# Performance work log

Hardware: AMD Instinct MI355X
Metric: run time of the kernel (lower is better)

Reference implementation:

```python
import jax, jax.numpy as jnp
import numpy as np
import math

N_HEADS = 8
NUM_LAYERS = 2
OUT_LEN = 96
MIN_FACTOR, MAX_FACTOR = 3, 10
MIN_KERNEL, MAX_KERNEL = 5, 51
LN_EPS = 1e-5


def layer_norm(x, g, b):
    mu = x.mean(-1, keepdims=True)
    var = x.var(-1, keepdims=True)  # biased, like nn.LayerNorm
    return (x - mu) / jnp.sqrt(var + LN_EPS) * g + b


def prob_sparse_attn(x, wq, bq, wk, bk, wv, bv, wo, bo):
    B, L, D = x.shape
    H, dk = N_HEADS, D // N_HEADS
    Q = (x @ wq + bq).reshape(B, L, H, dk).transpose(0, 2, 1, 3)  # [B,H,L,dk]
    K = (x @ wk + bk).reshape(B, L, H, dk).transpose(0, 2, 1, 3)
    V = (x @ wv + bv).reshape(B, L, H, dk).transpose(0, 2, 1, 3)
    # sparsity score per query: 0.5*||q|| + 0.3*entropy(softmax(q)) + 0.2*var(q)
    l2 = jnp.linalg.norm(Q, axis=-1)
    prob = jax.nn.softmax(Q, axis=-1)
    ent = -jnp.sum(prob * jnp.log(prob + 1e-9), axis=-1)
    var = Q.var(axis=-1, ddof=1)  # torch.var unbiased
    qs = 0.5 * l2 + 0.3 * ent + 0.2 * var  # [B,H,L]
    std = qs.std(axis=2, ddof=1)
    mean = qs.mean(axis=2)
    factor = jnp.clip(jnp.round(std / (mean + 1e-6) * MAX_FACTOR), MIN_FACTOR, MAX_FACTOR).astype(jnp.int32)  # [B,H]
    u = factor[:, 0]  # torch uses k_list[b][0]: head-0 factor per batch
    umax = min(MAX_FACTOR, L)
    _, top_idx = jax.lax.top_k(qs, umax)  # [B,H,umax]
    keep = jnp.arange(umax)[None, None, :] < u[:, None, None]  # [B,1->H,umax]
    Qs = jnp.take_along_axis(Q, top_idx[..., None], axis=2)  # [B,H,umax,dk]
    scores = jnp.einsum('bhud,bhld->bhul', Qs, K) / math.sqrt(dk)
    attn = jax.nn.softmax(scores, axis=-1)
    out = jnp.einsum('bhul,bhld->bhud', attn, V)  # [B,H,umax,dk]
    # scatter selected query outputs back; rows beyond u[b] are dropped (OOB index L)
    idx = jnp.where(keep, top_idx, L)
    full = jnp.zeros((B, H, L, dk), x.dtype)
    bI = jnp.arange(B)[:, None, None]
    hI = jnp.arange(H)[None, :, None]
    full = full.at[bI, hI, idx].set(out, mode='drop')
    y = full.transpose(0, 2, 1, 3).reshape(B, L, D)
    return y @ wo + bo


def adaptive_decomp(x):
    B, L, D = x.shape
    spec = jnp.abs(jnp.fft.rfft(x, axis=1)).mean(axis=(0, 2))
    peak = jnp.argmax(spec[1:]) + 1
    period = jnp.clip(L // peak, MIN_KERNEL, MAX_KERNEL)
    period = jnp.where(period % 2 == 0, period + 1, period)
    pad = period // 2
    # avg_pool1d(kernel=period, stride=1, padding=pad, count_include_pad=False) via cumsum
    t = jnp.arange(L)
    start = jnp.clip(t - pad, 0, L)
    end = jnp.clip(t + pad + 1, 0, L)
    cs = jnp.concatenate([jnp.zeros((B, 1, D), x.dtype), jnp.cumsum(x, axis=1)], axis=1)
    cnt = (end - start).astype(x.dtype)[None, :, None]
    trend = (cs[:, end] - cs[:, start]) / cnt
    return x - trend, trend


def _forward(x, w_embed, b_embed, wq, bq, wk, bk, wv, bv, wo, bo,
             w1, b1, w2, b2, g1, beta1, g2, beta2, w_out, b_out):
    h = x @ w_embed + b_embed
    for _ in range(NUM_LAYERS):  # share_params=True: same weights each layer
        a = prob_sparse_attn(h, wq, bq, wk, bk, wv, bv, wo, bo)
        h = layer_norm(h + a, g1, beta1)
        ffn = jax.nn.relu(h @ w1 + b1) @ w2 + b2
        h = layer_norm(h + ffn, g2, beta2)
    seasonal, trend = adaptive_decomp(h)
    combined = seasonal + trend
    out_seq = combined[:, -OUT_LEN:, :]
    pred = (out_seq @ w_out + b_out)[..., 0]  # [B, OUT_LEN]
    return pred


def setup_inputs() -> dict:
    key = jax.random.key(0)
    ks = jax.random.split(key, 16)
    B, L, Din, D, Dff = 16, 4096, 8, 512, 2048
    w = lambda k, shp: (jax.random.normal(k, shp, jnp.float32) * 0.02)
    return {
        'x': jax.random.normal(ks[0], (B, L, Din), jnp.float32),
        'w_embed': w(ks[1], (Din, D)), 'b_embed': jnp.zeros((D,), jnp.float32),
        'wq': w(ks[2], (D, D)), 'bq': jnp.zeros((D,), jnp.float32),
        'wk': w(ks[3], (D, D)), 'bk': jnp.zeros((D,), jnp.float32),
        'wv': w(ks[4], (D, D)), 'bv': jnp.zeros((D,), jnp.float32),
        'wo': w(ks[5], (D, D)), 'bo': jnp.zeros((D,), jnp.float32),
        'w1': w(ks[6], (D, Dff)), 'b1': jnp.zeros((Dff,), jnp.float32),
        'w2': w(ks[7], (Dff, D)), 'b2': jnp.zeros((D,), jnp.float32),
        'g1': jnp.ones((D,), jnp.float32), 'beta1': jnp.zeros((D,), jnp.float32),
        'g2': jnp.ones((D,), jnp.float32), 'beta2': jnp.zeros((D,), jnp.float32),
        'w_out': w(ks[8], (D, 1)), 'b_out': jnp.zeros((1,), jnp.float32),
    }


def reference(x, w_embed, b_embed, wq, bq, wk, bk, wv, bv, wo, bo,
              w1, b1, w2, b2, g1, beta1, g2, beta2, w_out, b_out):
    return _forward(x, w_embed, b_embed, wq, bq, wk, bk, wv, bv, wo, bo,
                    w1, b1, w2, b2, g1, beta1, g2, beta2, w_out, b_out)
```

## Files before the change

### kernel.cpp

```cpp
#include <hip/hip_runtime.h>
#include <math.h>

#define BB 16
#define LL 4096
#define DIN 8
#define DD 512
#define HH 8
#define DKK 64
#define DFF 2048
#define OUTLEN 96
#define TAIL0 (LL - OUTLEN)
#define NTAIL (BB * OUTLEN)
#define UMAX 10
#define CH 8192
#define QKVN 1536
#define NB 4
#define QM (NB * LL)
#define NSPLIT 32
#define LCHUNK (LL / NSPLIT)
#define PSTRIDE 68
#define MAXSLOT 128

typedef unsigned short ushort_t;
typedef unsigned int uint_t;
typedef short bf16x8 __attribute__((ext_vector_type(8)));
typedef float f32x4 __attribute__((ext_vector_type(4)));

#define GLD16(gp, lp) __builtin_amdgcn_global_load_lds((const __attribute__((address_space(1))) void*)(gp), (__attribute__((address_space(3))) void*)(lp), 16, 0, 0)

__device__ inline float wsum(float v){
#pragma unroll
  for (int o = 32; o > 0; o >>= 1) v += __shfl_xor(v, o);
  return v;
}
__device__ inline float wmax(float v){
#pragma unroll
  for (int o = 32; o > 0; o >>= 1) v = fmaxf(v, __shfl_xor(v, o));
  return v;
}
__device__ inline ushort_t f2bf_rtn(float f){
  uint_t u = __float_as_uint(f);
  uint_t r = u + 0x7FFF + ((u >> 16) & 1);
  return (ushort_t)(r >> 16);
}
__device__ inline float bf2f(ushort_t u){
  return __uint_as_float(((uint_t)u) << 16);
}
__device__ inline void split2(float x, ushort_t& hi, ushort_t& lo){
  uint_t u = __float_as_uint(x);
  hi = (ushort_t)(u >> 16);
  lo = f2bf_rtn(x - __uint_as_float(u & 0xFFFF0000u));
}

__global__ __launch_bounds__(256) void embed_kernel(const float* __restrict__ x,
    const float* __restrict__ we, const float* __restrict__ be,
    ushort_t* __restrict__ hh, ushort_t* __restrict__ hl){
  int row = blockIdx.x;
  __shared__ float xs[DIN];
  if (threadIdx.x < DIN) xs[threadIdx.x] = x[(size_t)row * DIN + threadIdx.x];
  __syncthreads();
  for (int j = threadIdx.x; j < DD; j += 256){
    float acc = be[j];
#pragma unroll
    for (int i = 0; i < DIN; ++i) acc += xs[i] * we[i * DD + j];
    ushort_t hu, lu; split2(acc, hu, lu);
    hh[(size_t)row * DD + j] = hu;
    hl[(size_t)row * DD + j] = lu;
  }
}

__global__ __launch_bounds__(256) void wsplit_t_kernel(const float* __restrict__ W,
    ushort_t* __restrict__ Th, ushort_t* __restrict__ Tl, int K, int N){
  int idx = blockIdx.x * 256 + threadIdx.x;
  if (idx >= N * K) return;
  int n = idx / K, k = idx - n * K;
  ushort_t hi, lo;
  split2(W[(size_t)k * N + n], hi, lo);
  Th[idx] = hi; Tl[idx] = lo;
}
__global__ __launch_bounds__(256) void wqkv_prep_kernel(const float* __restrict__ wq,
    const float* __restrict__ wk, const float* __restrict__ wv,
    ushort_t* __restrict__ Th, ushort_t* __restrict__ Tl){
  int idx = blockIdx.x * 256 + threadIdx.x;
  if (idx >= QKVN * DD) return;
  int n = idx >> 9, k = idx & (DD - 1);
  const float* src = (n < 512) ? wq : (n < 1024) ? wk : wv;
  ushort_t hi, lo;
  split2(src[(size_t)k * DD + (n & 511)], hi, lo);
  Th[idx] = hi; Tl[idx] = lo;
}
__global__ __launch_bounds__(256) void bqkv_prep_kernel(const float* __restrict__ bq,
    const float* __restrict__ bk, const float* __restrict__ bv, float* __restrict__ bo_){
  int n = blockIdx.x * 256 + threadIdx.x;
  if (n >= QKVN) return;
  bo_[n] = (n < 512) ? bq[n] : (n < 1024) ? bk[n - 512] : bv[n - 1024];
}

__global__ __launch_bounds__(256) void gemm_qkv(
    const ushort_t* __restrict__ Ah, const ushort_t* __restrict__ Al,
    const ushort_t* __restrict__ Bh, const ushort_t* __restrict__ Bl,
    const float* __restrict__ bias, float* __restrict__ Q,
    ushort_t* __restrict__ KV){
  __shared__ __align__(16) ushort_t AsH[128 * 32];
  __shared__ __align__(16) ushort_t AsL[128 * 32];
  __shared__ __align__(16) ushort_t BsH[128 * 32];
  __shared__ __align__(16) ushort_t BsL[128 * 32];
  const int tid  = threadIdx.x;
  const int lane = tid & 63;
  const int wv   = tid >> 6;
  const int m0   = blockIdx.y * 128;
  const int n0   = blockIdx.x * 128;
  const bool isQ = (n0 < 512);
  const int wm   = (wv & 1) * 64;
  const int wn   = (wv >> 1) * 64;

  const int rowA = tid >> 2;
  const int qe   = (tid & 3) * 8;
  const int lds0 = tid * 8;
  const int lds1 = (tid + 256) * 8;

  f32x4 acc[4][4];
#pragma unroll
  for (int i = 0; i < 4; ++i)
#pragma unroll
    for (int j = 0; j < 4; ++j) acc[i][j] = (f32x4){0.f, 0.f, 0.f, 0.f};

  const int arow = lane & 15;
  const int koff = (lane >> 4) * 8;
  const int K = DD;

  for (int k0 = 0; k0 < K; k0 += 32){
    const size_t ga0 = (size_t)(m0 + rowA) * K + k0 + qe;
    const size_t ga1 = (size_t)(m0 + rowA + 64) * K + k0 + qe;
    const size_t gb0 = (size_t)(n0 + rowA) * K + k0 + qe;
    const size_t gb1 = (size_t)(n0 + rowA + 64) * K + k0 + qe;
    GLD16(Ah + ga0, &AsH[lds0]);  GLD16(Ah + ga1, &AsH[lds1]);
    GLD16(Al + ga0, &AsL[lds0]);  GLD16(Al + ga1, &AsL[lds1]);
    GLD16(Bh + gb0, &BsH[lds0]);  GLD16(Bh + gb1, &BsH[lds1]);
    if (isQ){ GLD16(Bl + gb0, &BsL[lds0]);  GLD16(Bl + gb1, &BsL[lds1]); }
    __syncthreads();

    bf16x8 ah[4], al[4], bh[4], bl[4];
#pragma unroll
    for (int i = 0; i < 4; ++i){
      ah[i] = *(const bf16x8*)&AsH[(wm + i * 16 + arow) * 32 + koff];
      al[i] = *(const bf16x8*)&AsL[(wm + i * 16 + arow) * 32 + koff];
      bh[i] = *(const bf16x8*)&BsH[(wn + i * 16 + arow) * 32 + koff];
      if (isQ) bl[i] = *(const bf16x8*)&BsL[(wn + i * 16 + arow) * 32 + koff];
    }
#pragma unroll
    for (int i = 0; i < 4; ++i)
#pragma unroll
      for (int j = 0; j < 4; ++j){
        acc[i][j] = __builtin_amdgcn_mfma_f32_16x16x32_bf16(ah[i], bh[j], acc[i][j], 0, 0, 0);
        acc[i][j] = __builtin_amdgcn_mfma_f32_16x16x32_bf16(al[i], bh[j], acc[i][j], 0, 0, 0);
        if (isQ)
          acc[i][j] = __builtin_amdgcn_mfma_f32_16x16x32_bf16(ah[i], bl[j], acc[i][j], 0, 0, 0);
      }
    __syncthreads();
  }

  const int crow = (lane >> 4) * 4;
  const int ccol = lane & 15;
#pragma unroll
  for (int i = 0; i < 4; ++i){
    const int gr0 = m0 + wm + i * 16 + crow;
#pragma unroll
    for (int j = 0; j < 4; ++j){
      const int gc = n0 + wn + j * 16 + ccol;
      const float bvv = bias[gc];
#pragma unroll
      for (int r = 0; r < 4; ++r){
        float v = acc[i][j][r] + bvv;
        const int gr = gr0 + r;
        if (isQ) Q[(size_t)gr * 512 + gc] = v;
        else     KV[(size_t)gr * 1024 + (gc - 512)] = f2bf_rtn(v);
      }
    }
  }
}

__global__ __launch_bounds__(256) void gemm_ffn1(
    const ushort_t* __restrict__ Ah, const ushort_t* __restrict__ Al,
    const ushort_t* __restrict__ Bh, const float* __restrict__ bias,
    ushort_t* __restrict__ Chid){
  __shared__ __align__(16) ushort_t AsH[128 * 32];
  __shared__ __align__(16) ushort_t AsL[128 * 32];
  __shared__ __align__(16) ushort_t BsH[128 * 32];
  const int tid  = threadIdx.x;
  const int lane = tid & 63;
  const int wv   = tid >> 6;
  const int m0   = blockIdx.y * 128;
  const int n0   = blockIdx.x * 128;
  const int wm   = (wv & 1) * 64;
  const int wn   = (wv >> 1) * 64;
  const int rowA = tid >> 2;
  const int qe   = (tid & 3) * 8;
  const int lds0 = tid * 8;
  const int lds1 = (tid + 256) * 8;

  f32x4 acc[4][4];
#pragma unroll
  for (int i = 0; i < 4; ++i)
#pragma unroll
    for (int j = 0; j < 4; ++j) acc[i][j] = (f32x4){0.f, 0.f, 0.f, 0.f};

  const int arow = lane & 15;
  const int koff = (lane >> 4) * 8;
  const int K = DD;

  for (int k0 = 0; k0 < K; k0 += 32){
    const size_t ga0 = (size_t)(m0 + rowA) * K + k0 + qe;
    const size_t ga1 = (size_t)(m0 + rowA + 64) * K + k0 + qe;
    const size_t gb0 = (size_t)(n0 + rowA) * K + k0 + qe;
    const size_t gb1 = (size_t)(n0 + rowA + 64) * K + k0 + qe;
    GLD16(Ah + ga0, &AsH[lds0]);  GLD16(Ah + ga1, &AsH[lds1]);
    GLD16(Al + ga0, &AsL[lds0]);  GLD16(Al + ga1, &AsL[lds1]);
    GLD16(Bh + gb0, &BsH[lds0]);  GLD16(Bh + gb1, &BsH[lds1]);
    __syncthreads();

    bf16x8 ah[4], al[4], bh[4];
#pragma unroll
    for (int i = 0; i < 4; ++i){
      ah[i] = *(const bf16x8*)&AsH[(wm + i * 16 + arow) * 32 + koff];
      al[i] = *(const bf16x8*)&AsL[(wm + i * 16 + arow) * 32 + koff];
      bh[i] = *(const bf16x8*)&BsH[(wn + i * 16 + arow) * 32 + koff];
    }
#pragma unroll
    for (int i = 0; i < 4; ++i)
#pragma unroll
      for (int j = 0; j < 4; ++j){
        acc[i][j] = __builtin_amdgcn_mfma_f32_16x16x32_bf16(ah[i], bh[j], acc[i][j], 0, 0, 0);
        acc[i][j] = __builtin_amdgcn_mfma_f32_16x16x32_bf16(al[i], bh[j], acc[i][j], 0, 0, 0);
      }
    __syncthreads();
  }

  const int crow = (lane >> 4) * 4;
  const int ccol = lane & 15;
#pragma unroll
  for (int i = 0; i < 4; ++i){
    const int gr0 = m0 + wm + i * 16 + crow;
#pragma unroll
    for (int j = 0; j < 4; ++j){
      const int gc = n0 + wn + j * 16 + ccol;
      const float bvv = bias[gc];
#pragma unroll
      for (int r = 0; r < 4; ++r){
        float v = fmaxf(acc[i][j][r] + bvv, 0.f);
        Chid[(size_t)(gr0 + r) * DFF + gc] = f2bf_rtn(v);
      }
    }
  }
}

__global__ __launch_bounds__(256) void gemm_ffn2(
    const ushort_t* __restrict__ Ahid,
    const ushort_t* __restrict__ Bh, const ushort_t* __restrict__ Bl,
    float* __restrict__ pbuf, size_t pstr){
  __shared__ __align__(16) ushort_t AsH[128 * 32];
  __shared__ __align__(16) ushort_t BsH[128 * 32];
  __shared__ __align__(16) ushort_t BsL[128 * 32];
  const int tid  = threadIdx.x;
  const int lane = tid & 63;
  const int wv   = tid >> 6;
  const int nblk = (int)blockIdx.x >> 1;
  const int kq   = (int)blockIdx.x & 1;
  const int m0   = blockIdx.y * 128;
  const int n0   = nblk * 128;
  const int wm   = (wv & 1) * 64;
  const int wn   = (wv >> 1) * 64;
  const int rowA = tid >> 2;
  const int qe   = (tid & 3) * 8;
  const int lds0 = tid * 8;
  const int lds1 = (tid + 256) * 8;

  f32x4 acc[4][4];
#pragma unroll
  for (int i = 0; i < 4; ++i)
#pragma unroll
    for (int j = 0; j < 4; ++j) acc[i][j] = (f32x4){0.f, 0.f, 0.f, 0.f};

  const int arow = lane & 15;
  const int koff = (lane >> 4) * 8;
  const int K = DFF;
  const int kper = K / 2;
  const int kbeg = kq * kper;

  for (int k0 = kbeg; k0 < kbeg + kper; k0 += 32){
    const size_t ga0 = (size_t)(m0 + rowA) * K + k0 + qe;
    const size_t ga1 = (size_t)(m0 + rowA + 64) * K + k0 + qe;
    const size_t gb0 = (size_t)(n0 + rowA) * K + k0 + qe;
    const size_t gb1 = (size_t)(n0 + rowA + 64) * K + k0 + qe;
    GLD16(Ahid + ga0, &AsH[lds0]);  GLD16(Ahid + ga1, &AsH[lds1]);
    GLD16(Bh + gb0, &BsH[lds0]);    GLD16(Bh + gb1, &BsH[lds1]);
    GLD16(Bl + gb0, &BsL[lds0]);    GLD16(Bl + gb1, &BsL[lds1]);
    __syncthreads();

    bf16x8 ah[4], bh[4], bl[4];
#pragma unroll
    for (int i = 0; i < 4; ++i){
      ah[i] = *(const bf16x8*)&AsH[(wm + i * 16 + arow) * 32 + koff];
      bh[i] = *(const bf16x8*)&BsH[(wn + i * 16 + arow) * 32 + koff];
      bl[i] = *(const bf16x8*)&BsL[(wn + i * 16 + arow) * 32 + koff];
    }
#pragma unroll
    for (int i = 0; i < 4; ++i)
#pragma unroll
      for (int j = 0; j < 4; ++j){
        acc[i][j] = __builtin_amdgcn_mfma_f32_16x16x32_bf16(ah[i], bh[j], acc[i][j], 0, 0, 0);
        acc[i][j] = __builtin_amdgcn_mfma_f32_16x16x32_bf16(ah[i], bl[j], acc[i][j], 0, 0, 0);
      }
    __syncthreads();
  }

  const int crow = (lane >> 4) * 4;
  const int ccol = lane & 15;
#pragma unroll
  for (int i = 0; i < 4; ++i){
    const int gr0 = m0 + wm + i * 16 + crow;
#pragma unroll
    for (int j = 0; j < 4; ++j){
      const int gc = n0 + wn + j * 16 + ccol;
#pragma unroll
      for (int r = 0; r < 4; ++r)
        pbuf[(size_t)kq * pstr + (size_t)(gr0 + r) * DD + gc] = acc[i][j][r];
    }
  }
}

__global__ __launch_bounds__(256) void qs_kernel(const float* __restrict__ qbuf, float* __restrict__ qsb){
  int tid = threadIdx.x;
  int lane = tid & 63;
  int wv = tid >> 6;
  int rid = blockIdx.x * 4 + wv;
  int bloc = rid >> 15;
  int hh = (rid >> 12) & 7;
  int l  = rid & (LL - 1);
  float qv = qbuf[((size_t)bloc * LL + l) * DD + hh * DKK + lane];
  float l2 = sqrtf(wsum(qv * qv));
  float mx = wmax(qv);
  float e  = expf(qv - mx);
  float se = wsum(e);
  float p  = e / se;
  float ent = -wsum(p * logf(p + 1e-9f));
  float mu  = wsum(qv) * (1.0f / 64.0f);
  float dv  = qv - mu;
  float var = wsum(dv * dv) * (1.0f / 63.0f);
  float val = 0.5f * l2 + 0.3f * ent + 0.2f * var;
  if (lane == 0) qsb[(size_t)(bloc * HH + hh) * LL + l] = val;
}

__global__ __launch_bounds__(256) void select_kernel(const float* __restrict__ qsb,
    int* __restrict__ topidx, int* __restrict__ ufac, int qtr){
  __shared__ float vals[LL];
  __shared__ float bv[256];
  __shared__ int   bi[256];
  __shared__ double r1[256], r2[256];
  const int bloc = blockIdx.y;
  const int b = qtr * NB + bloc;
  int tid = threadIdx.x;
  if (blockIdx.x == 8){
    const float* row = qsb + (size_t)bloc * HH * LL;
    double s = 0.0, s2 = 0.0;
    for (int l = tid; l < LL; l += 256){ double v = row[l]; s += v; s2 += v * v; }
    r1[tid] = s; r2[tid] = s2; __syncthreads();
    for (int st = 128; st; st >>= 1){
      if (tid < st){ r1[tid] += r1[tid+st]; r2[tid] += r2[tid+st]; }
      __syncthreads();
    }
    if (tid == 0){
      double mean = r1[0] / (double)LL;
      double var  = (r2[0] - (double)LL * mean * mean) / (double)(LL - 1);
      if (var < 0.0) var = 0.0;
      double f = rint(sqrt(var) / (mean + 1e-6) * 10.0);
      if (f < 3.0) f = 3.0;
      if (f > 10.0) f = 10.0;
      ufac[b] = (int)f;
    }
    return;
  }
  int hh = blockIdx.x;
  const float* row = qsb + ((size_t)bloc * HH + hh) * LL;
  for (int l = tid; l < LL; l += 256) vals[l] = row[l];
  __syncthreads();
  for (int it = 0; it < UMAX; ++it){
    float best = -INFINITY; int bidx = 0;
    for (int l = tid; l < LL; l += 256){
      float v = vals[l];
      if (v > best){ best = v; bidx = l; }
    }
    bv[tid] = best; bi[tid] = bidx; __syncthreads();
    for (int st = 128; st; st >>= 1){
      if (tid < st){
        if (bv[tid+st] > bv[tid] || (bv[tid+st] == bv[tid] && bi[tid+st] < bi[tid])){
          bv[tid] = bv[tid+st]; bi[tid] = bi[tid+st];
        }
      }
      __syncthreads();
    }
    if (tid == 0){ topidx[(b * HH + hh) * UMAX + it] = bi[0]; vals[bi[0]] = -INFINITY; }
    __syncthreads();
  }
}

__global__ void initslot_kernel(int* __restrict__ slotmap, int* __restrict__ scount){
  int i = blockIdx.x * 256 + threadIdx.x;
  if (i < BB * LL) slotmap[i] = -1;
  if (i < BB) scount[i] = 0;
}
__global__ __launch_bounds__(128) void slotbuild_kernel(const int* __restrict__ topidx,
    const int* __restrict__ ufac, int* __restrict__ slotmap, int* __restrict__ scount, int qtr){
  int t = threadIdx.x;
  int b = qtr * NB + blockIdx.x;
  if (t >= HH * UMAX) return;
  int hh = t / UMAX, rank = t % UMAX;
  if (rank >= ufac[b]) return;
  int qpos = topidx[(b * HH + hh) * UMAX + rank];
  int* cell = &slotmap[b * LL + qpos];
  int old = atomicCAS(cell, -1, -2);
  if (old == -1){
    int s = atomicAdd(&scount[b], 1);
    atomicExch(cell, s);
  }
}

__global__ __launch_bounds__(256) void attn_p1_kernel(const float* __restrict__ qbuf,
    const ushort_t* __restrict__ kvbuf,
    const int* __restrict__ topidx, const int* __restrict__ ufac,
    float* __restrict__ part, int qtr, int lmin){
  const int bloc = blockIdx.z;
  const int b = qtr * NB + bloc;
  const int rowid = blockIdx.y;
  const int hh = rowid / UMAX, rank = rowid % UMAX;
  if (rank >= ufac[b]) return;
  const int qpos = topidx[(b * HH + hh) * UMAX + rank];
  if (qpos < lmin) return;

  const int tid = threadIdx.x, lane = tid & 63, wv = tid >> 6;
  const int base = blockIdx.x * LCHUNK + wv * (LCHUNK / 4);

  __shared__ float qrow[DKK];
  __shared__ float wm4[4], ws4[4];
  __shared__ float pvs[4][DKK];
  if (tid < DKK) qrow[tid] = qbuf[((size_t)bloc * LL + qpos) * DD + hh * DKK + tid];
  __syncthreads();

  const ushort_t* Kp = kvbuf + (size_t)bloc * LL * 1024 + hh * DKK;
  const ushort_t* Vp = Kp + 512;
  const float qv = qrow[lane];

  float sc[32];
  float mloc = -INFINITY;
#pragma unroll
  for (int i = 0; i < 32; ++i){
    float s = wsum(qv * bf2f(Kp[(size_t)(base + i) * 1024 + lane])) * 0.125f;
    sc[i] = s;
    mloc = fmaxf(mloc, s);
  }
  if (lane == 0) wm4[wv] = mloc;
  __syncthreads();
  const float M4 = fmaxf(fmaxf(wm4[0], wm4[1]), fmaxf(wm4[2], wm4[3]));

  float ssum = 0.f;
#pragma unroll
  for (int i = 0; i < 32; ++i){ float e = expf(sc[i] - M4); sc[i] = e; ssum += e; }

  float pv = 0.f;
#pragma unroll
  for (int i = 0; i < 32; ++i) pv += sc[i] * bf2f(Vp[(size_t)(base + i) * 1024 + lane]);

  pvs[wv][lane] = pv;
  if (lane == 0) ws4[wv] = ssum;
  __syncthreads();
  if (wv == 0){
    float* rec = part + (size_t)((bloc * HH * UMAX + rowid) * NSPLIT + blockIdx.x) * PSTRIDE;
    rec[lane] = pvs[0][lane] + pvs[1][lane] + pvs[2][lane] + pvs[3][lane];
    if (lane == 0){ rec[64] = M4; rec[65] = ws4[0] + ws4[1] + ws4[2] + ws4[3]; }
  }
}

__global__ __launch_bounds__(256) void attn_p2_kernel(const float* __restrict__ part,
    const float* __restrict__ wo, const int* __restrict__ topidx, const int* __restrict__ ufac,
    const int* __restrict__ slotmap, float* __restrict__ adelta, int qtr, int lmin){
  const int bloc = blockIdx.y;
  const int b = qtr * NB + bloc;
  const int rowid = blockIdx.x;
  const int hh = rowid / UMAX, rank = rowid % UMAX;
  if (rank >= ufac[b]) return;
  const int qpos = topidx[(b * HH + hh) * UMAX + rank];
  if (qpos < lmin) return;
  const int slot = slotmap[b * LL + qpos];

  const int tid = threadIdx.x;
  const float* pbase = part + (size_t)(bloc * HH * UMAX + rowid) * NSPLIT * PSTRIDE;
  __shared__ float pm[NSPLIT], ps[NSPLIT];
  __shared__ float orow[DKK];
  if (tid < NSPLIT){
    pm[tid] = pbase[(size_t)tid * PSTRIDE + 64];
    ps[tid] = pbase[(size_t)tid * PSTRIDE + 65];
  }
  __syncthreads();
  float M = -INFINITY;
#pragma unroll
  for (int i = 0; i < NSPLIT; ++i) M = fmaxf(M, pm[i]);
  float S = 0.f;
#pragma unroll
  for (int i = 0; i < NSPLIT; ++i) S += ps[i] * expf(pm[i] - M);
  if (tid < DKK){
    float acc = 0.f;
#pragma unroll
    for (int i = 0; i < NSPLIT; ++i)
      acc += pbase[(size_t)i * PSTRIDE + tid] * expf(pm[i] - M);
    orow[tid] = acc / S;
  }
  __syncthreads();
  float* drow = adelta + ((size_t)b * MAXSLOT + slot) * DD;
  for (int j = tid; j < DD; j += 256){
    float a = 0.f;
#pragma unroll
    for (int dd = 0; dd < DKK; ++dd) a += orow[dd] * wo[(size_t)(hh * DKK + dd) * DD + j];
    atomicAdd(&drow[j], a);
  }
}

__global__ void zero_kernel(float* __restrict__ p, size_t n){
  size_t i = (size_t)blockIdx.x * 256 + threadIdx.x;
  size_t stride = (size_t)gridDim.x * 256;
  for (; i < n; i += stride) p[i] = 0.f;
}

template<bool TAIL>
__global__ __launch_bounds__(256) void ln1_kernel(
    const ushort_t* __restrict__ hh_, const ushort_t* __restrict__ hl_,
    const float* __restrict__ bo,
    const int* __restrict__ slotmap, const float* __restrict__ adelta,
    ushort_t* __restrict__ oh, ushort_t* __restrict__ ol,
    const float* __restrict__ g, const float* __restrict__ bb){
  __shared__ float red[256];
  int r = blockIdx.x, tid = threadIdx.x;
  int b, l;
  if (TAIL){ b = r / OUTLEN; l = TAIL0 + (r % OUTLEN); }
  else     { b = r >> 12;    l = r & (LL - 1); }
  const size_t gi = ((size_t)b * LL + l) * DD;
  float v0 = bf2f(hh_[gi + tid])       + bf2f(hl_[gi + tid])       + bo[tid];
  float v1 = bf2f(hh_[gi + tid + 256]) + bf2f(hl_[gi + tid + 256]) + bo[tid + 256];
  int s = slotmap[b * LL + l];
  if (s >= 0){
    const float* dr = adelta + ((size_t)b * MAXSLOT + s) * DD;
    v0 += dr[tid]; v1 += dr[tid + 256];
  }
  red[tid] = v0 + v1; __syncthreads();
  for (int st = 128; st; st >>= 1){ if (tid < st) red[tid] += red[tid+st]; __syncthreads(); }
  float mu = red[0] * (1.0f / DD); __syncthreads();
  float d0 = v0 - mu, d1 = v1 - mu;
  red[tid] = d0*d0 + d1*d1; __syncthreads();
  for (int st = 128; st; st >>= 1){ if (tid < st) red[tid] += red[tid+st]; __syncthreads(); }
  float rstd = rsqrtf(red[0] * (1.0f / DD) + 1e-5f);
  float o0 = d0 * rstd * g[tid]       + bb[tid];
  float o1 = d1 * rstd * g[tid + 256] + bb[tid + 256];
  const size_t oo = TAIL ? (size_t)r * DD : gi;
  ushort_t hu, lu;
  split2(o0, hu, lu); oh[oo + tid] = hu;       ol[oo + tid] = lu;
  split2(o1, hu, lu); oh[oo + tid + 256] = hu; ol[oo + tid + 256] = lu;
}

template<bool TAIL>
__global__ __launch_bounds__(256) void ln2_kernel(
    const ushort_t* __restrict__ ih, const ushort_t* __restrict__ il,
    const float* __restrict__ pbuf, size_t pstr, const float* __restrict__ b2,
    ushort_t* __restrict__ oh, ushort_t* __restrict__ ol, float* __restrict__ ofp,
    const float* __restrict__ g, const float* __restrict__ bb, size_t rowoff){
  __shared__ float red[256];
  int r = blockIdx.x, tid = threadIdx.x;
  const size_t gi = (rowoff + r) * DD;
  const size_t pi = (size_t)r * DD;
  float v0 = bf2f(ih[gi + tid]) + bf2f(il[gi + tid])
           + pbuf[pi + tid] + pbuf[pstr + pi + tid] + b2[tid];
  float v1 = bf2f(ih[gi + tid + 256]) + bf2f(il[gi + tid + 256])
           + pbuf[pi + tid + 256] + pbuf[pstr + pi + tid + 256] + b2[tid + 256];
  red[tid] = v0 + v1; __syncthreads();
  for (int st = 128; st; st >>= 1){ if (tid < st) red[tid] += red[tid+st]; __syncthreads(); }
  float mu = red[0] * (1.0f / DD); __syncthreads();
  float d0 = v0 - mu, d1 = v1 - mu;
  red[tid] = d0*d0 + d1*d1; __syncthreads();
  for (int st = 128; st; st >>= 1){ if (tid < st) red[tid] += red[tid+st]; __syncthreads(); }
  float rstd = rsqrtf(red[0] * (1.0f / DD) + 1e-5f);
  float o0 = d0 * rstd * g[tid]       + bb[tid];
  float o1 = d1 * rstd * g[tid + 256] + bb[tid + 256];
  if (TAIL){
    ofp[pi + tid] = o0; ofp[pi + tid + 256] = o1;
  } else {
    ushort_t hu, lu;
    split2(o0, hu, lu); oh[gi + tid] = hu;       ol[gi + tid] = lu;
    split2(o1, hu, lu); oh[gi + tid + 256] = hu; ol[gi + tid + 256] = lu;
  }
}

__global__ __launch_bounds__(64) void pred_kernel(const float* __restrict__ ht,
    const float* __restrict__ wout, const float* __restrict__ bout, float* __restrict__ out){
  int r = blockIdx.x, lane = threadIdx.x;
  float acc = 0.f;
  for (int dd = lane; dd < DD; dd += 64) acc += ht[(size_t)r * DD + dd] * wout[dd];
  acc = wsum(acc);
  if (lane == 0) out[r] = acc + bout[0];
}

extern "C" void kernel_launch(void* const* d_in, const int* in_sizes, int n_in,
                              void* d_out, int out_size, void* d_ws, size_t ws_size,
                              hipStream_t stream){
  const float* x    = (const float*)d_in[0];
  const float* wemb = (const float*)d_in[1];
  const float* bemb = (const float*)d_in[2];
  const float* wq   = (const float*)d_in[3];
  const float* bq   = (const float*)d_in[4];
  const float* wk   = (const float*)d_in[5];
  const float* bk   = (const float*)d_in[6];
  const float* wv   = (const float*)d_in[7];
  const float* bvv  = (const float*)d_in[8];
  const float* wo   = (const float*)d_in[9];
  const float* bo   = (const float*)d_in[10];
  const float* w1   = (const float*)d_in[11];
  const float* b1   = (const float*)d_in[12];
  const float* w2   = (const float*)d_in[13];
  const float* b2   = (const float*)d_in[14];
  const float* g1   = (const float*)d_in[15];
  const float* be1  = (const float*)d_in[16];
  const float* g2   = (const float*)d_in[17];
  const float* be2  = (const float*)d_in[18];
  const float* wout = (const float*)d_in[19];
  const float* bout = (const float*)d_in[20];
  float* out = (float*)d_out;
  char* wsb  = (char*)d_ws;

  const size_t MiB = 1024 * 1024;
  const size_t NE  = (size_t)BB * LL * DD;

  size_t o = 0;
  ushort_t* hh    = (ushort_t*)(wsb + o); o += NE * 2;
  ushort_t* hl    = (ushort_t*)(wsb + o); o += NE * 2;
  char*     arena = wsb + o;              o += 64 * MiB;
  float*    qbuf  = (float*)arena;
  ushort_t* kvbuf = (ushort_t*)(arena + 32 * MiB);
  ushort_t* hid   = (ushort_t*)arena;
  float*    pbuf  = (float*)(arena + 32 * MiB);
  ushort_t* hidt  = (ushort_t*)arena;
  float*    pbuft = (float*)(arena + 32 * MiB);
  ushort_t* asht  = (ushort_t*)(arena + 48 * MiB);
  ushort_t* aslt  = (ushort_t*)(arena + 50 * MiB);
  ushort_t* wtqkvh = (ushort_t*)(wsb + o); o += (size_t)QKVN * DD * 2;
  ushort_t* wtqkvl = (ushort_t*)(wsb + o); o += (size_t)QKVN * DD * 2;
  ushort_t* w1th   = (ushort_t*)(wsb + o); o += (size_t)DFF * DD * 2;
  ushort_t* w2th   = (ushort_t*)(wsb + o); o += (size_t)DD * DFF * 2;
  ushort_t* w2tl   = (ushort_t*)(wsb + o); o += (size_t)DD * DFF * 2;
  ushort_t* w1tl   = (ushort_t*)(wsb + o); o += (size_t)DFF * DD * 2;
  float*    bqkv   = (float*)(wsb + o);  o += QKVN * 4;
  float*    qsb    = (float*)(wsb + o);  o += (size_t)NB * HH * LL * 4;
  float*    part   = (float*)(wsb + o);  o += (size_t)NB * HH * UMAX * NSPLIT * PSTRIDE * 4;
  float*    adelta = (float*)(wsb + o);  o += (size_t)BB * MAXSLOT * DD * 4;
  float*    htail  = (float*)(wsb + o);  o += (size_t)NTAIL * DD * 4;
  int*      slotmap= (int*)(wsb + o);    o += (size_t)BB * LL * 4;
  int*      scount = (int*)(wsb + o);    o += BB * 4;
  int*      topidx = (int*)(wsb + o);    o += (size_t)BB * HH * UMAX * 4;
  int*      ufac   = (int*)(wsb + o);    o += 64;

  wqkv_prep_kernel<<<(QKVN*DD + 255)/256, 256, 0, stream>>>(wq, wk, wv, wtqkvh, wtqkvl);
  bqkv_prep_kernel<<<(QKVN + 255)/256, 256, 0, stream>>>(bq, bk, bvv, bqkv);
  wsplit_t_kernel<<<(DFF*DD + 255)/256, 256, 0, stream>>>(w1, w1th, w1tl, DD, DFF);
  wsplit_t_kernel<<<(DD*DFF + 255)/256, 256, 0, stream>>>(w2, w2th, w2tl, DFF, DD);

  embed_kernel<<<BB * LL, 256, 0, stream>>>(x, wemb, bemb, hh, hl);

  for (int layer = 0; layer < 2; ++layer){
    const bool tail = (layer == 1);
    const int lmin = tail ? TAIL0 : 0;

    initslot_kernel<<<(BB*LL + 255)/256, 256, 0, stream>>>(slotmap, scount);
    zero_kernel<<<1024, 256, 0, stream>>>(adelta, (size_t)BB * MAXSLOT * DD);

    for (int qtr = 0; qtr < BB / NB; ++qtr){
      const size_t hoff = (size_t)qtr * QM * DD;
      gemm_qkv<<<dim3(QKVN/128, QM/128), 256, 0, stream>>>(
          hh + hoff, hl + hoff, wtqkvh, wtqkvl, bqkv, qbuf, kvbuf);
      qs_kernel<<<(NB*HH*LL)/4, 256, 0, stream>>>(qbuf, qsb);
      select_kernel<<<dim3(9, NB), 256, 0, stream>>>(qsb, topidx, ufac, qtr);
      slotbuild_kernel<<<NB, 128, 0, stream>>>(topidx, ufac, slotmap, scount, qtr);
      attn_p1_kernel<<<dim3(NSPLIT, HH*UMAX, NB), 256, 0, stream>>>(
          qbuf, kvbuf, topidx, ufac, part, qtr, lmin);
      attn_p2_kernel<<<dim3(HH*UMAX, NB), 256, 0, stream>>>(
          part, wo, topidx, ufac, slotmap, adelta, qtr, lmin);
    }

    if (!tail){
      ln1_kernel<false><<<BB*LL, 256, 0, stream>>>(hh, hl, bo, slotmap, adelta, hh, hl, g1, be1);
      for (int c = 0; c < (BB*LL)/CH; ++c){
        const size_t roff = (size_t)c * CH;
        gemm_ffn1<<<dim3(DFF/128, CH/128), 256, 0, stream>>>(
            hh + roff * DD, hl + roff * DD, w1th, b1, hid);
        gemm_ffn2<<<dim3(8, CH/128), 256, 0, stream>>>(hid, w2th, w2tl, pbuf, (size_t)CH * DD);
        ln2_kernel<false><<<CH, 256, 0, stream>>>(
            hh, hl, pbuf, (size_t)CH * DD, b2, hh, hl, nullptr, g2, be2, roff);
      }
    } else {
      ln1_kernel<true><<<NTAIL, 256, 0, stream>>>(hh, hl, bo, slotmap, adelta, asht, aslt, g1, be1);
      gemm_ffn1<<<dim3(DFF/128, NTAIL/128), 256, 0, stream>>>(asht, aslt, w1th, b1, hidt);
      gemm_ffn2<<<dim3(8, NTAIL/128), 256, 0, stream>>>(hidt, w2th, w2tl, pbuft, (size_t)NTAIL * DD);
      ln2_kernel<true><<<NTAIL, 256, 0, stream>>>(
          asht, aslt, pbuft, (size_t)NTAIL * DD, b2, nullptr, nullptr, htail, g2, be2, 0);
      pred_kernel<<<NTAIL, 64, 0, stream>>>(htail, wout, bout, out);
    }
  }
  (void)in_sizes; (void)n_in; (void)out_size; (void)ws_size;
}
```

Measured before the change: 2.583 ms.

## Add XCD-aware block swizzle, reuse K/V across queries, vectorize LN and embed

Adds an XCD-aware workgroup remapping to the three GEMM kernels so neighbouring tiles share the same L2 on the MI355X's multiple compute dies. The attention partial kernel now loads each head's K/V chunk into registers once and loops over the selected query ranks, instead of launching one block per rank that re-reads K/V. The top-k selection keeps per-thread running maxima and rescans only the thread that owned the removed element, avoiding a full rescan per iteration. LayerNorm and embed kernels switch to packed 2-element loads and stores. The costs are more register pressure in the attention kernel and serialization across ranks inside a block.

```diff
diff --git a/kernel.cpp b/kernel.cpp
--- a/kernel.cpp
+++ b/kernel.cpp
@@ -51,6 +51,15 @@
   hi = (ushort_t)(u >> 16);
   lo = f2bf_rtn(x - __uint_as_float(u & 0xFFFF0000u));
 }
+__device__ inline void xcd_map(int& bx, int& by){
+  const int gx = gridDim.x;
+  const int nwg = gx * gridDim.y;
+  const int wg = (int)blockIdx.y * gx + (int)blockIdx.x;
+  const int q = nwg >> 3, r = nwg & 7;
+  const int xcd = wg & 7, idx = wg >> 3;
+  const int swz = (xcd < r ? xcd * (q + 1) : r * (q + 1) + (xcd - r) * q) + idx;
+  bx = swz % gx; by = swz / gx;
+}
 
 __global__ __launch_bounds__(256) void embed_kernel(const float* __restrict__ x,
     const float* __restrict__ we, const float* __restrict__ be,
@@ -59,14 +68,18 @@
   __shared__ float xs[DIN];
   if (threadIdx.x < DIN) xs[threadIdx.x] = x[(size_t)row * DIN + threadIdx.x];
   __syncthreads();
-  for (int j = threadIdx.x; j < DD; j += 256){
-    float acc = be[j];
-#pragma unroll
-    for (int i = 0; i < DIN; ++i) acc += xs[i] * we[i * DD + j];
-    ushort_t hu, lu; split2(acc, hu, lu);
-    hh[(size_t)row * DD + j] = hu;
-    hl[(size_t)row * DD + j] = lu;
-  }
+  const int t = threadIdx.x;
+  const int j0 = 2 * t;
+  float a0 = be[j0], a1 = be[j0 + 1];
+#pragma unroll
+  for (int i = 0; i < DIN; ++i){
+    a0 += xs[i] * we[i * DD + j0];
+    a1 += xs[i] * we[i * DD + j0 + 1];
+  }
+  ushort_t h0, l0, h1, l1;
+  split2(a0, h0, l0); split2(a1, h1, l1);
+  ((uint_t*)(hh + (size_t)row * DD))[t] = (uint_t)h0 | ((uint_t)h1 << 16);
+  ((uint_t*)(hl + (size_t)row * DD))[t] = (uint_t)l0 | ((uint_t)l1 << 16);
 }
 
 __global__ __launch_bounds__(256) void wsplit_t_kernel(const float* __restrict__ W,
@@ -105,11 +118,12 @@
   __shared__ __align__(16) ushort_t AsL[128 * 32];
   __shared__ __align__(16) ushort_t BsH[128 * 32];
   __shared__ __align__(16) ushort_t BsL[128 * 32];
+  int bx, by; xcd_map(bx, by);
   const int tid  = threadIdx.x;
   const int lane = tid & 63;
   const int wv   = tid >> 6;
-  const int m0   = blockIdx.y * 128;
-  const int n0   = blockIdx.x * 128;
+  const int m0   = by * 128;
+  const int n0   = bx * 128;
   const bool isQ = (n0 < 512);
   const int wm   = (wv & 1) * 64;
   const int wn   = (wv >> 1) * 64;
@@ -187,11 +201,12 @@
   __shared__ __align__(16) ushort_t AsH[128 * 32];
   __shared__ __align__(16) ushort_t AsL[128 * 32];
   __shared__ __align__(16) ushort_t BsH[128 * 32];
+  int bx, by; xcd_map(bx, by);
   const int tid  = threadIdx.x;
   const int lane = tid & 63;
   const int wv   = tid >> 6;
-  const int m0   = blockIdx.y * 128;
-  const int n0   = blockIdx.x * 128;
+  const int m0   = by * 128;
+  const int n0   = bx * 128;
   const int wm   = (wv & 1) * 64;
   const int wn   = (wv >> 1) * 64;
   const int rowA = tid >> 2;
@@ -261,12 +276,13 @@
   __shared__ __align__(16) ushort_t AsH[128 * 32];
   __shared__ __align__(16) ushort_t BsH[128 * 32];
   __shared__ __align__(16) ushort_t BsL[128 * 32];
+  int bx, by; xcd_map(bx, by);
   const int tid  = threadIdx.x;
   const int lane = tid & 63;
   const int wv   = tid >> 6;
-  const int nblk = (int)blockIdx.x >> 1;
-  const int kq   = (int)blockIdx.x & 1;
-  const int m0   = blockIdx.y * 128;
+  const int nblk = bx >> 1;
+  const int kq   = bx & 1;
+  const int m0   = by * 128;
   const int n0   = nblk * 128;
   const int wm   = (wv & 1) * 64;
   const int wn   = (wv >> 1) * 64;
@@ -356,6 +372,7 @@
   __shared__ float vals[LL];
   __shared__ float bv[256];
   __shared__ int   bi[256];
+  __shared__ int   widx_s;
   __shared__ double r1[256], r2[256];
   const int bloc = blockIdx.y;
   const int b = qtr * NB + bloc;
@@ -384,13 +401,14 @@
   const float* row = qsb + ((size_t)bloc * HH + hh) * LL;
   for (int l = tid; l < LL; l += 256) vals[l] = row[l];
   __syncthreads();
+  float lmax = -INFINITY; int lidx = 0;
+  for (int l = tid; l < LL; l += 256){
+    float v = vals[l];
+    if (v > lmax){ lmax = v; lidx = l; }
+  }
   for (int it = 0; it < UMAX; ++it){
-    float best = -INFINITY; int bidx = 0;
-    for (int l = tid; l < LL; l += 256){
-      float v = vals[l];
-      if (v > best){ best = v; bidx = l; }
-    }
-    bv[tid] = best; bi[tid] = bidx; __syncthreads();
+    bv[tid] = lmax; bi[tid] = lidx;
+    __syncthreads();
     for (int st = 128; st; st >>= 1){
       if (tid < st){
         if (bv[tid+st] > bv[tid] || (bv[tid+st] == bv[tid] && bi[tid+st] < bi[tid])){
@@ -399,7 +417,17 @@
       }
       __syncthreads();
     }
-    if (tid == 0){ topidx[(b * HH + hh) * UMAX + it] = bi[0]; vals[bi[0]] = -INFINITY; }
+    if (tid == 0){ topidx[(b * HH + hh) * UMAX + it] = bi[0]; widx_s = bi[0]; }
+    __syncthreads();
+    const int w = widx_s;
+    if ((w & 255) == tid){
+      vals[w] = -INFINITY;
+      lmax = -INFINITY; lidx = 0;
+      for (int l = tid; l < LL; l += 256){
+        float v = vals[l];
+        if (v > lmax){ lmax = v; lidx = l; }
+      }
+    }
     __syncthreads();
   }
 }
@@ -431,52 +459,58 @@
     float* __restrict__ part, int qtr, int lmin){
   const int bloc = blockIdx.z;
   const int b = qtr * NB + bloc;
-  const int rowid = blockIdx.y;
-  const int hh = rowid / UMAX, rank = rowid % UMAX;
-  if (rank >= ufac[b]) return;
-  const int qpos = topidx[(b * HH + hh) * UMAX + rank];
-  if (qpos < lmin) return;
-
+  const int hh = blockIdx.y;
+  const int u = ufac[b];
   const int tid = threadIdx.x, lane = tid & 63, wv = tid >> 6;
-  const int base = blockIdx.x * LCHUNK + wv * (LCHUNK / 4);
-
-  __shared__ float qrow[DKK];
+  const int base = blockIdx.x * LCHUNK + wv * 32;
+
+  const ushort_t* Kp = kvbuf + (size_t)bloc * LL * 1024 + hh * DKK + lane;
+  const ushort_t* Vp = Kp + 512;
+  float kreg[32], vreg[32];
+#pragma unroll
+  for (int i = 0; i < 32; ++i){
+    kreg[i] = bf2f(Kp[(size_t)(base + i) * 1024]);
+    vreg[i] = bf2f(Vp[(size_t)(base + i) * 1024]);
+  }
+
   __shared__ float wm4[4], ws4[4];
   __shared__ float pvs[4][DKK];
-  if (tid < DKK) qrow[tid] = qbuf[((size_t)bloc * LL + qpos) * DD + hh * DKK + tid];
-  __syncthreads();
-
-  const ushort_t* Kp = kvbuf + (size_t)bloc * LL * 1024 + hh * DKK;
-  const ushort_t* Vp = Kp + 512;
-  const float qv = qrow[lane];
-
-  float sc[32];
-  float mloc = -INFINITY;
-#pragma unroll
-  for (int i = 0; i < 32; ++i){
-    float s = wsum(qv * bf2f(Kp[(size_t)(base + i) * 1024 + lane])) * 0.125f;
-    sc[i] = s;
-    mloc = fmaxf(mloc, s);
-  }
-  if (lane == 0) wm4[wv] = mloc;
-  __syncthreads();
-  const float M4 = fmaxf(fmaxf(wm4[0], wm4[1]), fmaxf(wm4[2], wm4[3]));
-
-  float ssum = 0.f;
-#pragma unroll
-  for (int i = 0; i < 32; ++i){ float e = expf(sc[i] - M4); sc[i] = e; ssum += e; }
-
-  float pv = 0.f;
-#pragma unroll
-  for (int i = 0; i < 32; ++i) pv += sc[i] * bf2f(Vp[(size_t)(base + i) * 1024 + lane]);
-
-  pvs[wv][lane] = pv;
-  if (lane == 0) ws4[wv] = ssum;
-  __syncthreads();
-  if (wv == 0){
-    float* rec = part + (size_t)((bloc * HH * UMAX + rowid) * NSPLIT + blockIdx.x) * PSTRIDE;
-    rec[lane] = pvs[0][lane] + pvs[1][lane] + pvs[2][lane] + pvs[3][lane];
-    if (lane == 0){ rec[64] = M4; rec[65] = ws4[0] + ws4[1] + ws4[2] + ws4[3]; }
+
+  for (int rank = 0; rank < u; ++rank){
+    const int qpos = topidx[(b * HH + hh) * UMAX + rank];
+    if (qpos < lmin) continue;
+    const float qv = qbuf[((size_t)bloc * LL + qpos) * DD + hh * DKK + lane];
+
+    float sc[32];
+    float mloc = -INFINITY;
+#pragma unroll
+    for (int i = 0; i < 32; ++i){
+      float s = wsum(qv * kreg[i]) * 0.125f;
+      sc[i] = s;
+      mloc = fmaxf(mloc, s);
+    }
+    if (lane == 0) wm4[wv] = mloc;
+    __syncthreads();
+    const float M4 = fmaxf(fmaxf(wm4[0], wm4[1]), fmaxf(wm4[2], wm4[3]));
+
+    float ssum = 0.f;
+#pragma unroll
+    for (int i = 0; i < 32; ++i){ float e = expf(sc[i] - M4); sc[i] = e; ssum += e; }
+
+    float pv = 0.f;
+#pragma unroll
+    for (int i = 0; i < 32; ++i) pv += sc[i] * vreg[i];
+
+    pvs[wv][lane] = pv;
+    if (lane == 0) ws4[wv] = ssum;
+    __syncthreads();
+    if (wv == 0){
+      const int rowid = hh * UMAX + rank;
+      float* rec = part + (size_t)((bloc * HH * UMAX + rowid) * NSPLIT + blockIdx.x) * PSTRIDE;
+      rec[lane] = pvs[0][lane] + pvs[1][lane] + pvs[2][lane] + pvs[3][lane];
+      if (lane == 0){ rec[64] = M4; rec[65] = ws4[0] + ws4[1] + ws4[2] + ws4[3]; }
+    }
+    __syncthreads();
   }
 }
 
@@ -543,12 +577,16 @@
   if (TAIL){ b = r / OUTLEN; l = TAIL0 + (r % OUTLEN); }
   else     { b = r >> 12;    l = r & (LL - 1); }
   const size_t gi = ((size_t)b * LL + l) * DD;
-  float v0 = bf2f(hh_[gi + tid])       + bf2f(hl_[gi + tid])       + bo[tid];
-  float v1 = bf2f(hh_[gi + tid + 256]) + bf2f(hl_[gi + tid + 256]) + bo[tid + 256];
+  const int j0 = 2 * tid;
+  const uint_t hp = *(const uint_t*)(hh_ + gi + j0);
+  const uint_t lp = *(const uint_t*)(hl_ + gi + j0);
+  const float2 bo2 = *(const float2*)&bo[j0];
+  float v0 = bf2f((ushort_t)(hp & 0xFFFF)) + bf2f((ushort_t)(lp & 0xFFFF)) + bo2.x;
+  float v1 = bf2f((ushort_t)(hp >> 16))    + bf2f((ushort_t)(lp >> 16))    + bo2.y;
   int s = slotmap[b * LL + l];
   if (s >= 0){
-    const float* dr = adelta + ((size_t)b * MAXSLOT + s) * DD;
-    v0 += dr[tid]; v1 += dr[tid + 256];
+    const float2 dr = *(const float2*)&adelta[((size_t)b * MAXSLOT + s) * DD + j0];
+    v0 += dr.x; v1 += dr.y;
   }
   red[tid] = v0 + v1; __syncthreads();
   for (int st = 128; st; st >>= 1){ if (tid < st) red[tid] += red[tid+st]; __syncthreads(); }
@@ -557,12 +595,15 @@
   red[tid] = d0*d0 + d1*d1; __syncthreads();
   for (int st = 128; st; st >>= 1){ if (tid < st) red[tid] += red[tid+st]; __syncthreads(); }
   float rstd = rsqrtf(red[0] * (1.0f / DD) + 1e-5f);
-  float o0 = d0 * rstd * g[tid]       + bb[tid];
-  float o1 = d1 * rstd * g[tid + 256] + bb[tid + 256];
+  const float2 g2 = *(const float2*)&g[j0];
+  const float2 bb2 = *(const float2*)&bb[j0];
+  float o0 = d0 * rstd * g2.x + bb2.x;
+  float o1 = d1 * rstd * g2.y + bb2.y;
   const size_t oo = TAIL ? (size_t)r * DD : gi;
-  ushort_t hu, lu;
-  split2(o0, hu, lu); oh[oo + tid] = hu;       ol[oo + tid] = lu;
-  split2(o1, hu, lu); oh[oo + tid + 256] = hu; ol[oo + tid + 256] = lu;
+  ushort_t h0, l0, h1, l1;
+  split2(o0, h0, l0); split2(o1, h1, l1);
+  *(uint_t*)(oh + oo + j0) = (uint_t)h0 | ((uint_t)h1 << 16);
+  *(uint_t*)(ol + oo + j0) = (uint_t)l0 | ((uint_t)l1 << 16);
 }
 
 template<bool TAIL>
@@ -575,10 +616,14 @@
   int r = blockIdx.x, tid = threadIdx.x;
   const size_t gi = (rowoff + r) * DD;
   const size_t pi = (size_t)r * DD;
-  float v0 = bf2f(ih[gi + tid]) + bf2f(il[gi + tid])
-           + pbuf[pi + tid] + pbuf[pstr + pi + tid] + b2[tid];
-  float v1 = bf2f(ih[gi + tid + 256]) + bf2f(il[gi + tid + 256])
-           + pbuf[pi + tid + 256] + pbuf[pstr + pi + tid + 256] + b2[tid + 256];
+  const int j0 = 2 * tid;
+  const uint_t hp = *(const uint_t*)(ih + gi + j0);
+  const uint_t lp = *(const uint_t*)(il + gi + j0);
+  const float2 p0 = *(const float2*)&pbuf[pi + j0];
+  const float2 p1 = *(const float2*)&pbuf[pstr + pi + j0];
+  const float2 b22 = *(const float2*)&b2[j0];
+  float v0 = bf2f((ushort_t)(hp & 0xFFFF)) + bf2f((ushort_t)(lp & 0xFFFF)) + p0.x + p1.x + b22.x;
+  float v1 = bf2f((ushort_t)(hp >> 16))    + bf2f((ushort_t)(lp >> 16))    + p0.y + p1.y + b22.y;
   red[tid] = v0 + v1; __syncthreads();
   for (int st = 128; st; st >>= 1){ if (tid < st) red[tid] += red[tid+st]; __syncthreads(); }
   float mu = red[0] * (1.0f / DD); __syncthreads();
@@ -586,14 +631,17 @@
   red[tid] = d0*d0 + d1*d1; __syncthreads();
   for (int st = 128; st; st >>= 1){ if (tid < st) red[tid] += red[tid+st]; __syncthreads(); }
   float rstd = rsqrtf(red[0] * (1.0f / DD) + 1e-5f);
-  float o0 = d0 * rstd * g[tid]       + bb[tid];
-  float o1 = d1 * rstd * g[tid + 256] + bb[tid + 256];
+  const float2 g2 = *(const float2*)&g[j0];
+  const float2 bb2 = *(const float2*)&bb[j0];
+  float o0 = d0 * rstd * g2.x + bb2.x;
+  float o1 = d1 * rstd * g2.y + bb2.y;
   if (TAIL){
-    ofp[pi + tid] = o0; ofp[pi + tid + 256] = o1;
+    ofp[pi + j0] = o0; ofp[pi + j0 + 1] = o1;
   } else {
-    ushort_t hu, lu;
-    split2(o0, hu, lu); oh[gi + tid] = hu;       ol[gi + tid] = lu;
-    split2(o1, hu, lu); oh[gi + tid + 256] = hu; ol[gi + tid + 256] = lu;
+    ushort_t h0, l0, h1, l1;
+    split2(o0, h0, l0); split2(o1, h1, l1);
+    *(uint_t*)(oh + gi + j0) = (uint_t)h0 | ((uint_t)h1 << 16);
+    *(uint_t*)(ol + gi + j0) = (uint_t)l0 | ((uint_t)l1 << 16);
   }
 }
 
@@ -685,7 +733,7 @@
       qs_kernel<<<(NB*HH*LL)/4, 256, 0, stream>>>(qbuf, qsb);
       select_kernel<<<dim3(9, NB), 256, 0, stream>>>(qsb, topidx, ufac, qtr);
       slotbuild_kernel<<<NB, 128, 0, stream>>>(topidx, ufac, slotmap, scount, qtr);
-      attn_p1_kernel<<<dim3(NSPLIT, HH*UMAX, NB), 256, 0, stream>>>(
+      attn_p1_kernel<<<dim3(NSPLIT, HH, NB), 256, 0, stream>>>(
           qbuf, kvbuf, topidx, ufac, part, qtr, lmin);
       attn_p2_kernel<<<dim3(HH*UMAX, NB), 256, 0, stream>>>(
           part, wo, topidx, ufac, slotmap, adelta, qtr, lmin);
```

New measurement: 2.549 ms. About the same (-1.3%).
